# Kernel optimization log

Measured on AMD Instinct MI355X. Metric: run time of the kernel, lower is better.

## Reference

```python
import jax, jax.numpy as jnp
import numpy as np

GROUPS = 8   # GroupNorm groups used by create_pat_conv*_blocks(..., groups=8)
EPS = 1e-5
K = 20       # num_neighbor


def group_norm(x, gamma, beta):
    # x: [B, C, ...spatial]
    B, C = x.shape[0], x.shape[1]
    shape = x.shape
    xg = x.reshape(B, GROUPS, C // GROUPS, -1)
    m = xg.mean(axis=(2, 3), keepdims=True)
    v = ((xg - m) ** 2).mean(axis=(2, 3), keepdims=True)
    xg = (xg - m) * jax.lax.rsqrt(v + EPS)
    x = xg.reshape(shape)
    bshape = (1, C) + (1,) * (len(shape) - 2)
    return x * gamma.reshape(bshape) + beta.reshape(bshape)


def conv_block(x, w, b, gamma, beta):
    # pointwise (kernel-size 1) conv + GroupNorm + ELU, works for 1d and 2d spatial
    y = jnp.einsum('oc,bc...->bo...', w, x) + b.reshape((1, -1) + (1,) * (x.ndim - 2))
    return jax.nn.elu(group_norm(y, gamma, beta))


def knn_graph(points, k):
    # points: [B, 3, N] -> neighbor coords [B, 3, N, k] (self included, dilation=1)
    sq = jnp.sum(points * points, axis=1)                      # [B, N]
    inner = jnp.einsum('bci,bcj->bij', points, points)         # [B, N, N]
    dist = sq[:, :, None] + sq[:, None, :] - 2.0 * inner       # squared pairwise dist
    _, idx = jax.lax.top_k(-dist, k)                           # [B, N, k] smallest dists
    neighbors = jnp.take_along_axis(points[:, :, None, :], idx[:, None, :, :], axis=3)
    return neighbors                                           # [B, 3, N, k]


def setup_inputs() -> dict:
    key = jax.random.key(0)
    B, N = 4, 8192
    dims1 = [6, 32, 64]
    dims2 = [64, 512, 1024]
    keys = iter(jax.random.split(key, 32))
    inp = {"points": jax.random.normal(next(keys), (B, 3, N), dtype=jnp.float32)}
    for tag, dims in (("p1", dims1), ("p2", dims2)):
        for i in range(len(dims) - 1):
            cin, cout = dims[i], dims[i + 1]
            inp[f"{tag}_w{i}"] = jax.random.normal(next(keys), (cout, cin), dtype=jnp.float32) / np.float32(np.sqrt(cin))
            inp[f"{tag}_b{i}"] = jnp.zeros((cout,), dtype=jnp.float32)
            inp[f"{tag}_g{i}"] = jnp.ones((cout,), dtype=jnp.float32)
            inp[f"{tag}_beta{i}"] = jnp.zeros((cout,), dtype=jnp.float32)
    return inp


def reference(points, p1_w0, p1_b0, p1_g0, p1_beta0, p1_w1, p1_b1, p1_g1, p1_beta1,
              p2_w0, p2_b0, p2_g0, p2_beta0, p2_w1, p2_b1, p2_g1, p2_beta1):
    neighbors = knn_graph(points, K)                             # [B, 3, N, K]
    center = jnp.broadcast_to(points[:, :, :, None], neighbors.shape)
    x = jnp.concatenate([center, neighbors - center], axis=1)   # [B, 6, N, K]
    x = conv_block(x, p1_w0, p1_b0, p1_g0, p1_beta0)            # [B, 32, N, K]
    x = conv_block(x, p1_w1, p1_b1, p1_g1, p1_beta1)            # [B, 64, N, K]
    x = jnp.max(x, axis=2)                                      # [B, 64, K] (faithful to source: max over dim=2)
    x = conv_block(x, p2_w0, p2_b0, p2_g0, p2_beta0)            # [B, 512, K]
    x = conv_block(x, p2_w1, p2_b1, p2_g1, p2_beta1)            # [B, 1024, K]
    return x
```

## Files before the change

### kernel.cpp

```cpp
#include <hip/hip_runtime.h>
#include <math.h>

#define NPTS   8192
#define BATCH  4
#define KNN    20
#define NKTOT  (NPTS*KNN)
#define EPS    1e-5f
#define QC2    16

#define WINW   3072
#define WITR   (WINW/4/128)
#define NBIN   1024
#define BIN_LO (-4.5f)
#define BIN_W  (9.0f/1024.0f)

typedef float v2f __attribute__((ext_vector_type(2)));

__device__ __forceinline__ float elu(float x) { return x > 0.0f ? x : expm1f(x); }
__device__ __forceinline__ float eluf(float x) { return x > 0.0f ? x : __expf(x) - 1.0f; }
__device__ __forceinline__ v2f splat2(float x) { v2f v; v.x = x; v.y = x; return v; }
__device__ __forceinline__ float rfl(float x) {
    return __uint_as_float(__builtin_amdgcn_readfirstlane(__float_as_uint(x)));
}

__device__ __forceinline__ unsigned fenc(float f) {
    unsigned b = __float_as_uint(f);
    return b ^ ((unsigned)(((int)b) >> 31) | 0x80000000u);
}
__device__ __forceinline__ float fdec(unsigned u) {
    unsigned b = (u & 0x80000000u) ? (u ^ 0x80000000u) : ~u;
    return __uint_as_float(b);
}

__device__ __forceinline__ int xbin(float x) {
    int bin = (int)floorf((x + 4.5f) * (1024.0f / 9.0f));
    return bin < 0 ? 0 : (bin > NBIN - 1 ? NBIN - 1 : bin);
}

__global__ __launch_bounds__(256) void prep_kernel(const float* __restrict__ points,
                                                   float4* __restrict__ pts4,
                                                   float* __restrict__ zeroreg,
                                                   unsigned* __restrict__ minenc,
                                                   unsigned* __restrict__ fcnt)
{
    const int t = blockIdx.x * 256 + threadIdx.x;
    const int b = t >> 13, n = t & (NPTS - 1);
    const float* px = points + b * 3 * NPTS;
    float x = px[n], y = px[NPTS + n], z = px[2 * NPTS + n];
    pts4[t] = make_float4(x, y, z, -0.5f * (x * x + y * y + z * z));
    if (t < 18176) zeroreg[t] = 0.f;
    if (t < 5120)  minenc[t] = 0xFFFFFFFFu;
    if (t < 4)     fcnt[t] = 0u;
}

__global__ __launch_bounds__(1024) void hist_kernel(const float* __restrict__ points,
                                                    int* __restrict__ Pcur)
{
    __shared__ int h[NBIN];
    __shared__ int sc[NBIN];
    const int b = blockIdx.x;
    const int t = threadIdx.x;
    h[t] = 0;
    __syncthreads();
    const float* px = points + b * 3 * NPTS;
    for (int i = t; i < NPTS; i += 1024)
        atomicAdd(&h[xbin(px[i])], 1);
    __syncthreads();
    int v = h[t];
    sc[t] = v;
    __syncthreads();
    for (int off = 1; off < NBIN; off <<= 1) {
        int a = (t >= off) ? sc[t - off] : 0;
        __syncthreads();
        sc[t] += a;
        __syncthreads();
    }
    Pcur[b * NBIN + t] = sc[t] - v;
}

__global__ __launch_bounds__(256) void scatter_kernel(const float4* __restrict__ pts4,
                                                      int* __restrict__ Pcur,
                                                      float4* __restrict__ psort,
                                                      int* __restrict__ sidx,
                                                      int* __restrict__ binof)
{
    const int t = blockIdx.x * 256 + threadIdx.x;
    const int b = t >> 13, n = t & (NPTS - 1);
    float4 p = pts4[t];
    int bin = xbin(p.x);
    int slot = atomicAdd(&Pcur[b * NBIN + bin], 1);
    psort[b * NPTS + slot] = p;
    sidx [b * NPTS + slot] = n;
    binof[b * NPTS + slot] = bin;
}

__global__ __launch_bounds__(256, 8) void knn_win_kernel(
    const float4* __restrict__ psort, const int* __restrict__ sidx,
    const int* __restrict__ binof, int* __restrict__ idx_out,
    unsigned* __restrict__ fcnt, int* __restrict__ flist)
{
    __shared__ unsigned long long queue[32][QC2];
    __shared__ float smaxs[4][8][64];
    __shared__ float gates[8];
    __shared__ int qcnt[32];

    const int tid  = threadIdx.x;
    const int lane = tid & 63;
    const int wv   = tid >> 6;
    const int b    = blockIdx.x >> 10;
    const int oct  = blockIdx.x & 1023;
    const int q0s  = oct * 8;
    const float4* psb = psort + b * NPTS;
    const int*    six = sidx  + b * NPTS;
    const int*    bob = binof + b * NPTS;

    int s = q0s + 4 - WINW / 2;
    if (s < 0) s = 0;
    if (s > NPTS - WINW) s = NPTS - WINW;

    if (tid < 32) qcnt[tid] = 0;

    float qx[8], qy[8], qz[8], q2[8];
    v2f smax2[8];
#pragma unroll
    for (int q = 0; q < 8; ++q) {
        float4 qp = psb[q0s + q];
        qx[q] = rfl(qp.x); qy[q] = rfl(qp.y); qz[q] = rfl(qp.z);
        q2[q] = rfl(-(qp.w + qp.w));
        smax2[q] = splat2(-INFINITY);
    }

    const int lbase = s + wv * 2 + lane * 8;

#pragma unroll 3
    for (int t = 0; t < WITR; ++t) {
        float4 p0 = psb[lbase + t * 512];
        float4 p1 = psb[lbase + t * 512 + 1];
        v2f px = { p0.x, p1.x }, py = { p0.y, p1.y };
        v2f pz = { p0.z, p1.z }, pw = { p0.w, p1.w };
#pragma unroll
        for (int q = 0; q < 8; ++q) {
            v2f sv = __builtin_elementwise_fma(splat2(qx[q]), px,
                     __builtin_elementwise_fma(splat2(qy[q]), py,
                     __builtin_elementwise_fma(splat2(qz[q]), pz, pw)));
            smax2[q] = __builtin_elementwise_max(smax2[q], sv);
        }
    }
#pragma unroll
    for (int q = 0; q < 8; ++q) smaxs[wv][q][lane] = fmaxf(smax2[q].x, smax2[q].y);
    __syncthreads();

#pragma unroll
    for (int qq = 0; qq < 2; ++qq) {
        const int q = wv * 2 + qq;
        float v = fmaxf(fmaxf(smaxs[0][q][lane], smaxs[1][q][lane]),
                        fmaxf(smaxs[2][q][lane], smaxs[3][q][lane]));
#pragma unroll
        for (int k = 2; k <= 64; k <<= 1)
#pragma unroll
            for (int j = k >> 1; j >= 1; j >>= 1) {
                float o = __shfl_xor(v, j);
                bool up = ((lane & k) == 0);
                bool keepmin = (((lane & j) == 0) == up);
                v = keepmin ? fminf(v, o) : fmaxf(v, o);
            }
        float m = __shfl(v, 44);
        if (lane == 0) gates[q] = m - 1e-4f - 1e-5f * fabsf(m);
    }
    __syncthreads();
    float sgate[8];
#pragma unroll
    for (int q = 0; q < 8; ++q) sgate[q] = gates[q];

    for (int t = 0; t < WITR; ++t) {
        const int jb = lbase + t * 512;
        float4 p0 = psb[jb];
        float4 p1 = psb[jb + 1];
        v2f px = { p0.x, p1.x }, py = { p0.y, p1.y };
        v2f pz = { p0.z, p1.z }, pw = { p0.w, p1.w };
#pragma unroll
        for (int q = 0; q < 8; ++q) {
            v2f sv = __builtin_elementwise_fma(splat2(qx[q]), px,
                     __builtin_elementwise_fma(splat2(qy[q]), py,
                     __builtin_elementwise_fma(splat2(qz[q]), pz, pw)));
            if (fmaxf(sv.x, sv.y) >= sgate[q]) {
#pragma unroll
                for (int h = 0; h < 2; ++h) {
                    float svh = h ? sv.y : sv.x;
                    if (svh >= sgate[q]) {
                        int slot = atomicAdd(&qcnt[wv * 8 + q], 1);
                        if (slot < QC2) {
                            int j = six[jb + h];
                            queue[wv * 8 + q][slot] =
                                ((unsigned long long)fenc(svh) << 32)
                                | (unsigned)(NPTS - 1 - j);
                        }
                    }
                }
            }
        }
    }
    __syncthreads();

    float xLe = (s == 0) ? -3.0e38f
                         : (BIN_LO + (float)(bob[s] + 1) * BIN_W);
    float xRe = (s == NPTS - WINW) ? 3.0e38f
                         : (BIN_LO + (float)bob[s + WINW] * BIN_W);

#pragma unroll
    for (int qq = 0; qq < 2; ++qq) {
        const int q = wv * 2 + qq;
        int c0r = qcnt[0 * 8 + q], c1r = qcnt[1 * 8 + q];
        int c2r = qcnt[2 * 8 + q], c3r = qcnt[3 * 8 + q];
        const bool ovf = (c0r > QC2) || (c1r > QC2) || (c2r > QC2) || (c3r > QC2);
        int c0 = c0r < QC2 ? c0r : QC2;
        int c1 = c1r < QC2 ? c1r : QC2;
        int c2 = c2r < QC2 ? c2r : QC2;
        int c3 = c3r < QC2 ? c3r : QC2;
        int b1 = c0, b2 = c0 + c1, b3 = c0 + c1 + c2, b4 = b3 + c3;
        unsigned long long key = 0ull;
        if (lane < b1)      key = queue[0 * 8 + q][lane];
        else if (lane < b2) key = queue[1 * 8 + q][lane - b1];
        else if (lane < b3) key = queue[2 * 8 + q][lane - b2];
        else if (lane < b4) key = queue[3 * 8 + q][lane - b3];
#pragma unroll
        for (int k = 2; k <= 64; k <<= 1)
#pragma unroll
            for (int j = k >> 1; j >= 1; j >>= 1) {
                unsigned long long o = __shfl_xor(key, j);
                bool up = ((lane & k) == 0);
                bool keepmax = (((lane & j) == 0) == up);
                bool omax = o > key;
                key = (keepmax == omax) ? o : key;
            }
        const int oq = __builtin_amdgcn_readfirstlane(six[q0s + q]);
        if (lane < KNN)
            idx_out[(b * KNN + lane) * NPTS + oq] =
                NPTS - 1 - (int)(unsigned)(key & 0xFFFFFFFFu);

        unsigned long long k19 = __shfl(key, 19);
        float s20 = fdec((unsigned)(k19 >> 32));
        float d20 = fmaxf(q2[q] - 2.0f * s20, 0.0f);
        float mg  = 1e-3f + 1e-3f * d20;
        float dL  = qx[q] - xLe;
        float dR  = xRe - qx[q];
        bool ok = !ovf && dL > 0.0f && dR > 0.0f
                  && (d20 + mg < dL * dL) && (d20 + mg < dR * dR);
        if (!ok && lane == 0) {
            unsigned fs = atomicAdd(&fcnt[b], 1u);
            if (fs < 8192u) flist[b * 8192 + fs] = oq;
        }
    }
}

__global__ __launch_bounds__(256, 8) void knn_fb_kernel(const float4* __restrict__ pts4,
                                                        int* __restrict__ idx_out,
                                                        const unsigned* __restrict__ fcnt,
                                                        const int* __restrict__ flist)
{
    __shared__ unsigned long long queue[32][QC2];
    __shared__ float smaxs[4][8][64];
    __shared__ float gates[8];
    __shared__ int qcnt[32];

    const int tid  = threadIdx.x;
    const int lane = tid & 63;
    const int wv   = tid >> 6;
    const int bb   = blockIdx.x & 3;
    unsigned cnt = fcnt[bb];
    if (cnt > 8192u) cnt = 8192u;
    const float4* pb = pts4 + bb * NPTS;
    const int* fl = flist + bb * 8192;
    const int cbase = wv * (NPTS / 4);
    const int tstep = gridDim.x >> 2;

    for (int task = blockIdx.x >> 2; task * 8 < (int)cnt; task += tstep) {
        int qn8[8];
        float qx[8], qy[8], qz[8];
        v2f smax2[8];
        if (tid < 32) qcnt[tid] = 0;
#pragma unroll
        for (int q = 0; q < 8; ++q) {
            int e = task * 8 + q;
            if (e >= (int)cnt) e = (int)cnt - 1;
            qn8[q] = __builtin_amdgcn_readfirstlane(fl[e]);
            float4 qp = pb[qn8[q]];
            qx[q] = rfl(qp.x); qy[q] = rfl(qp.y); qz[q] = rfl(qp.z);
            smax2[q] = splat2(-INFINITY);
        }

#pragma unroll 4
        for (int t = 0; t < NPTS / 4 / 128; ++t) {
            float4 p0 = pb[cbase + t * 128 + 2 * lane];
            float4 p1 = pb[cbase + t * 128 + 2 * lane + 1];
            v2f px = { p0.x, p1.x }, py = { p0.y, p1.y };
            v2f pz = { p0.z, p1.z }, pw = { p0.w, p1.w };
#pragma unroll
            for (int q = 0; q < 8; ++q) {
                v2f sv = __builtin_elementwise_fma(splat2(qx[q]), px,
                         __builtin_elementwise_fma(splat2(qy[q]), py,
                         __builtin_elementwise_fma(splat2(qz[q]), pz, pw)));
                smax2[q] = __builtin_elementwise_max(smax2[q], sv);
            }
        }
#pragma unroll
        for (int q = 0; q < 8; ++q) smaxs[wv][q][lane] = fmaxf(smax2[q].x, smax2[q].y);
        __syncthreads();

#pragma unroll
        for (int qq = 0; qq < 2; ++qq) {
            const int q = wv * 2 + qq;
            float v = fmaxf(fmaxf(smaxs[0][q][lane], smaxs[1][q][lane]),
                            fmaxf(smaxs[2][q][lane], smaxs[3][q][lane]));
#pragma unroll
            for (int k = 2; k <= 64; k <<= 1)
#pragma unroll
                for (int j = k >> 1; j >= 1; j >>= 1) {
                    float o = __shfl_xor(v, j);
                    bool up = ((lane & k) == 0);
                    bool keepmin = (((lane & j) == 0) == up);
                    v = keepmin ? fminf(v, o) : fmaxf(v, o);
                }
            float m = __shfl(v, 44);
            if (lane == 0) gates[q] = m - 1e-4f - 1e-5f * fabsf(m);
        }
        __syncthreads();
        float sgate[8];
#pragma unroll
        for (int q = 0; q < 8; ++q) sgate[q] = gates[q];

        for (int t = 0; t < NPTS / 4 / 128; ++t) {
            float4 p0 = pb[cbase + t * 128 + 2 * lane];
            float4 p1 = pb[cbase + t * 128 + 2 * lane + 1];
            v2f px = { p0.x, p1.x }, py = { p0.y, p1.y };
            v2f pz = { p0.z, p1.z }, pw = { p0.w, p1.w };
            const int jb = cbase + t * 128 + 2 * lane;
#pragma unroll
            for (int q = 0; q < 8; ++q) {
                v2f sv = __builtin_elementwise_fma(splat2(qx[q]), px,
                         __builtin_elementwise_fma(splat2(qy[q]), py,
                         __builtin_elementwise_fma(splat2(qz[q]), pz, pw)));
                if (fmaxf(sv.x, sv.y) >= sgate[q]) {
#pragma unroll
                    for (int h = 0; h < 2; ++h) {
                        float svh = h ? sv.y : sv.x;
                        if (svh >= sgate[q]) {
                            int slot = atomicAdd(&qcnt[wv * 8 + q], 1);
                            if (slot < QC2) {
                                unsigned long long key =
                                    ((unsigned long long)fenc(svh) << 32)
                                    | (unsigned)(NPTS - 1 - (jb + h));
                                queue[wv * 8 + q][slot] = key;
                            }
                        }
                    }
                }
            }
        }
        __syncthreads();

#pragma unroll
        for (int qq = 0; qq < 2; ++qq) {
            const int q = wv * 2 + qq;
            int c0 = qcnt[0 * 8 + q];  c0 = c0 < QC2 ? c0 : QC2;
            int c1 = qcnt[1 * 8 + q];  c1 = c1 < QC2 ? c1 : QC2;
            int c2 = qcnt[2 * 8 + q];  c2 = c2 < QC2 ? c2 : QC2;
            int c3 = qcnt[3 * 8 + q];  c3 = c3 < QC2 ? c3 : QC2;
            int b1 = c0, b2 = c0 + c1, b3 = c0 + c1 + c2, b4 = b3 + c3;
            unsigned long long key = 0ull;
            if (lane < b1)      key = queue[0 * 8 + q][lane];
            else if (lane < b2) key = queue[1 * 8 + q][lane - b1];
            else if (lane < b3) key = queue[2 * 8 + q][lane - b2];
            else if (lane < b4) key = queue[3 * 8 + q][lane - b3];
#pragma unroll
            for (int k = 2; k <= 64; k <<= 1)
#pragma unroll
                for (int j = k >> 1; j >= 1; j >>= 1) {
                    unsigned long long o = __shfl_xor(key, j);
                    bool up = ((lane & k) == 0);
                    bool keepmax = (((lane & j) == 0) == up);
                    bool omax = o > key;
                    key = (keepmax == omax) ? o : key;
                }
            if (lane < KNN)
                idx_out[(bb * KNN + lane) * NPTS + qn8[q]] =
                    NPTS - 1 - (int)(unsigned)(key & 0xFFFFFFFFu);
        }
        __syncthreads();
    }
}

__global__ __launch_bounds__(256) void moments_x_kernel(const float4* __restrict__ pts4,
                                                        const int* __restrict__ idx,
                                                        float* __restrict__ sums1p)
{
    const int b  = blockIdx.x / 80;
    const int r0 = (blockIdx.x - b * 80) * 2048;
    const float4* pb = pts4 + b * NPTS;
    const int* ib = idx + b * NKTOT;

    float v[27];
#pragma unroll
    for (int i = 0; i < 27; ++i) v[i] = 0.f;

    for (int e = 0; e < 8; ++e) {
        const int id = r0 + e * 256 + threadIdx.x;
        const int n = id & (NPTS - 1);
        const int j = ib[id];
        float4 c4 = pb[n];
        float4 e4 = pb[j];
        float x[6] = { c4.x, c4.y, c4.z, e4.x - c4.x, e4.y - c4.y, e4.z - c4.z };
        int p = 6;
#pragma unroll
        for (int d = 0; d < 6; ++d) {
            v[d] += x[d];
#pragma unroll
            for (int ee = d; ee < 6; ++ee) v[p++] += x[d] * x[ee];
        }
    }
#pragma unroll
    for (int i = 0; i < 27; ++i)
        for (int o = 32; o > 0; o >>= 1) v[i] += __shfl_xor(v[i], o);

    __shared__ float red[4][27];
    const int lane = threadIdx.x & 63, w = threadIdx.x >> 6;
    if (lane == 0)
#pragma unroll
        for (int i = 0; i < 27; ++i) red[w][i] = v[i];
    __syncthreads();
    if (threadIdx.x < 27) {
        float acc = red[0][threadIdx.x] + red[1][threadIdx.x] + red[2][threadIdx.x] + red[3][threadIdx.x];
        int slot = blockIdx.x & 63;
        atomicAdd(&sums1p[(slot * BATCH + b) * 27 + threadIdx.x], acc);
    }
}

__global__ void finalize1_kernel(const float* __restrict__ sums1p,
                                 const float* __restrict__ w1, const float* __restrict__ b1,
                                 const float* __restrict__ g1, const float* __restrict__ beta1,
                                 float* __restrict__ w1f)
{
    __shared__ float S[BATCH][27];
    const int t = threadIdx.x;
    if (t < 108) {
        int b = t / 27, i = t % 27;
        float acc = 0.f;
        for (int s = 0; s < 64; ++s) acc += sums1p[(s * BATCH + b) * 27 + i];
        S[b][i] = acc;
    }
    __syncthreads();
    const int b = t >> 5, c = t & 31;
    const float invS = 1.0f / (float)NKTOT;
    float Ex[6], M[6][6];
#pragma unroll
    for (int d = 0; d < 6; ++d) Ex[d] = S[b][d] * invS;
    int p = 6;
#pragma unroll
    for (int d = 0; d < 6; ++d)
#pragma unroll
        for (int e = d; e < 6; ++e) { float v = S[b][p++] * invS; M[d][e] = v; M[e][d] = v; }
    const int g = c >> 2;
    float msum = 0.f, qsum = 0.f;
    for (int cc = g * 4; cc < g * 4 + 4; ++cc) {
        float w[6];
#pragma unroll
        for (int d = 0; d < 6; ++d) w[d] = w1[cc * 6 + d];
        float dotEx = 0.f;
#pragma unroll
        for (int d = 0; d < 6; ++d) dotEx += w[d] * Ex[d];
        float Ey = dotEx + b1[cc];
        float Ey2 = 0.f;
#pragma unroll
        for (int d = 0; d < 6; ++d)
#pragma unroll
            for (int e = 0; e < 6; ++e) Ey2 += w[d] * w[e] * M[d][e];
        Ey2 += 2.0f * b1[cc] * dotEx + b1[cc] * b1[cc];
        msum += Ey; qsum += Ey2;
    }
    float m = msum * 0.25f;
    float var = qsum * 0.25f - m * m;
    float inv = rsqrtf(var + EPS);
    float s = g1[c] * inv;
    float tt = s * (b1[c] - m) + beta1[c];
    float* o = w1f + (b * 32 + c) * 8;
#pragma unroll
    for (int d = 0; d < 6; ++d) o[d] = s * w1[c * 6 + d];
    o[6] = tt; o[7] = 0.f;
}

__global__ __launch_bounds__(256, 3) void fused_main_kernel(
    const float4* __restrict__ pts4, const int* __restrict__ idxb,
    const float* __restrict__ w1f, const float* __restrict__ w2, const float* __restrict__ b2,
    float* __restrict__ sums2p, unsigned int* __restrict__ maxenc, unsigned int* __restrict__ minenc)
{
    __shared__ __align__(16) float w2t[32 * 64];
    __shared__ __align__(16) float z1s[32 * 256];
    __shared__ __align__(16) float4 w1s4[64];
    __shared__ float b2s[64];
    __shared__ float redmx[256], redmn[256], sqred[64];

    const int t   = threadIdx.x;
    const int blk = blockIdx.x;
    const int nc  = blk & 15;
    const int k   = (blk >> 4) % 20;
    const int b   = blk / 320;

    for (int i = t; i < 512; i += 256) {
        float4 v = ((const float4*)w2)[i];
        int c = i >> 3, kq = (i & 7) * 4;
        w2t[(kq + 0) * 64 + c] = v.x; w2t[(kq + 1) * 64 + c] = v.y;
        w2t[(kq + 2) * 64 + c] = v.z; w2t[(kq + 3) * 64 + c] = v.w;
    }
    if (t < 64) { w1s4[t] = ((const float4*)w1f)[b * 64 + t]; b2s[t] = b2[t]; }

    const int wvi = t >> 6;
    const int cg8 = t & 7;
    const int n0  = (t >> 3) * 8;
    const int c0  = cg8 * 8;
    const float4* pb = pts4 + b * NPTS;
    const int nbase = nc * 512;
    const int* idxrow = idxb + (b * KNN + k) * NPTS;

    float mx[8], mn[8];
#pragma unroll
    for (int ci = 0; ci < 8; ++ci) { mx[ci] = -INFINITY; mn[ci] = INFINITY; }
    float gs = 0.f, gq = 0.f;

    for (int ph = 0; ph < 2; ++ph) {
        const int n = nbase + ph * 256 + t;
        const int j = idxrow[n];
        float4 c4 = pb[n];
        float4 e4 = pb[j];
        float x0[6] = { c4.x, c4.y, c4.z, e4.x - c4.x, e4.y - c4.y, e4.z - c4.z };

        __syncthreads();
#pragma unroll
        for (int c = 0; c < 32; ++c) {
            float4 wA = w1s4[c * 2 + 0];
            float4 wB = w1s4[c * 2 + 1];
            float z = wB.z;
            z = fmaf(wA.x, x0[0], z); z = fmaf(wA.y, x0[1], z); z = fmaf(wA.z, x0[2], z);
            z = fmaf(wA.w, x0[3], z); z = fmaf(wB.x, x0[4], z); z = fmaf(wB.y, x0[5], z);
            z1s[c * 256 + t] = eluf(z);
        }
        __syncthreads();

        float acc[8][8];
#pragma unroll
        for (int ci = 0; ci < 8; ++ci) {
            float bb = b2s[c0 + ci];
#pragma unroll
            for (int pj = 0; pj < 8; ++pj) acc[ci][pj] = bb;
        }
#pragma unroll
        for (int kk = 0; kk < 32; ++kk) {
            float4 a0 = *(const float4*)&w2t[kk * 64 + c0];
            float4 a1 = *(const float4*)&w2t[kk * 64 + c0 + 4];
            float4 z0 = *(const float4*)&z1s[kk * 256 + n0];
            float4 z1v = *(const float4*)&z1s[kk * 256 + n0 + 4];
            float avv[8] = { a0.x, a0.y, a0.z, a0.w, a1.x, a1.y, a1.z, a1.w };
            float zvv[8] = { z0.x, z0.y, z0.z, z0.w, z1v.x, z1v.y, z1v.z, z1v.w };
#pragma unroll
            for (int ci = 0; ci < 8; ++ci)
#pragma unroll
                for (int pj = 0; pj < 8; ++pj) acc[ci][pj] = fmaf(avv[ci], zvv[pj], acc[ci][pj]);
        }
#pragma unroll
        for (int ci = 0; ci < 8; ++ci)
#pragma unroll
            for (int pj = 0; pj < 8; ++pj) {
                float v = acc[ci][pj];
                gs += v; gq = fmaf(v, v, gq);
                mx[ci] = fmaxf(mx[ci], v); mn[ci] = fminf(mn[ci], v);
            }
    }

#pragma unroll
    for (int m = 8; m <= 32; m <<= 1) {
#pragma unroll
        for (int ci = 0; ci < 8; ++ci) {
            mx[ci] = fmaxf(mx[ci], __shfl_xor(mx[ci], m));
            mn[ci] = fminf(mn[ci], __shfl_xor(mn[ci], m));
        }
        gs += __shfl_xor(gs, m);
        gq += __shfl_xor(gq, m);
    }
    if ((t & 63) < 8) {
        const int l = t & 7;
#pragma unroll
        for (int ci = 0; ci < 8; ++ci) {
            redmx[wvi * 64 + l * 8 + ci] = mx[ci];
            redmn[wvi * 64 + l * 8 + ci] = mn[ci];
        }
        sqred[(wvi * 8 + l) * 2 + 0] = gs;
        sqred[(wvi * 8 + l) * 2 + 1] = gq;
    }
    __syncthreads();
    if (t < 64) {
        float m = fmaxf(fmaxf(redmx[t], redmx[64 + t]), fmaxf(redmx[128 + t], redmx[192 + t]));
        atomicMax(&maxenc[(b * 64 + t) * KNN + k], fenc(m));
    } else if (t < 128) {
        int c = t - 64;
        float m = fminf(fminf(redmn[c], redmn[64 + c]), fminf(redmn[128 + c], redmn[192 + c]));
        atomicMin(&minenc[(b * 64 + c) * KNN + k], fenc(m));
    } else if (t < 144) {
        int i2 = t - 128, g = i2 >> 1, w = i2 & 1;
        float v = 0.f;
#pragma unroll
        for (int wv2 = 0; wv2 < 4; ++wv2)
            v += sqred[(wv2 * 8 + g) * 2 + w];
        int slot = blk & 63;
        atomicAdd(&sums2p[((slot * BATCH + b) * 8 + g) * 2 + w], v);
    }
}

__global__ void build_m1_kernel(const float* __restrict__ sums2p,
                                const unsigned int* __restrict__ maxenc,
                                const unsigned int* __restrict__ minenc,
                                const float* __restrict__ gamma, const float* __restrict__ beta,
                                float* __restrict__ m1)
{
    const int t = blockIdx.x * 256 + threadIdx.x;
    const int b = t / 1280;
    const int r = t - b * 1280;
    const int c = r / 20;
    const int g = c >> 3;
    float s = 0.f, q = 0.f;
    for (int sl = 0; sl < 64; ++sl) {
        s += sums2p[((sl * BATCH + b) * 8 + g) * 2 + 0];
        q += sums2p[((sl * BATCH + b) * 8 + g) * 2 + 1];
    }
    const float cnt = 8.0f * (float)NKTOT;
    float m = s / cnt;
    float var = q / cnt - m * m;
    float inv = rsqrtf(var + EPS);
    float sc = gamma[c] * inv;
    float tt = beta[c] - sc * m;
    float y = (sc >= 0.f) ? fdec(maxenc[t]) : fdec(minenc[t]);
    m1[t] = elu(sc * y + tt);
}

template <int CIN, int SLOTS>
__global__ void p2_gemm_kernel(const float* __restrict__ zin, const float* __restrict__ w,
                               const float* __restrict__ bias, float* __restrict__ yout,
                               float* __restrict__ sumsp, int chans_per_group)
{
    const int t = blockIdx.x * 256 + threadIdx.x;
    const int per_b = (gridDim.x * 256) / BATCH;
    const int b = t / per_b;
    const int r = t - b * per_b;
    const int o = r / 20;
    const int k = r - o * 20;
    const float* zb = zin + b * CIN * 20;
    const float* wrow = w + o * CIN;
    float acc = bias[o];
    for (int c = 0; c < CIN; c += 4) {
        float4 wv = *(const float4*)&wrow[c];
        acc += wv.x * zb[(c + 0) * 20 + k] + wv.y * zb[(c + 1) * 20 + k]
             + wv.z * zb[(c + 2) * 20 + k] + wv.w * zb[(c + 3) * 20 + k];
    }
    yout[t] = acc;

    __shared__ float ls[16];
    if (threadIdx.x < 16) ls[threadIdx.x] = 0.f;
    __syncthreads();
    const int g = o / chans_per_group;
    atomicAdd(&ls[g * 2 + 0], acc);
    atomicAdd(&ls[g * 2 + 1], acc * acc);
    __syncthreads();
    if (threadIdx.x < 16) {
        int slot = blockIdx.x & (SLOTS - 1);
        atomicAdd(&sumsp[(slot * BATCH + b) * 16 + threadIdx.x], ls[threadIdx.x]);
    }
}

template <int SLOTS>
__global__ void p2_finalize_kernel(const float* __restrict__ y, const float* __restrict__ sumsp,
                                   const float* __restrict__ gamma, const float* __restrict__ beta,
                                   float* __restrict__ z, int chans_per_group, float cnt)
{
    const int t = blockIdx.x * 256 + threadIdx.x;
    const int per_b = (gridDim.x * 256) / BATCH;
    const int b = t / per_b;
    const int r = t - b * per_b;
    const int o = r / 20;
    const int g = o / chans_per_group;
    float s = 0.f, q = 0.f;
    for (int sl = 0; sl < SLOTS; ++sl) {
        s += sumsp[(sl * BATCH + b) * 16 + g * 2 + 0];
        q += sumsp[(sl * BATCH + b) * 16 + g * 2 + 1];
    }
    float m = s / cnt;
    float var = q / cnt - m * m;
    float inv = rsqrtf(var + EPS);
    float v = gamma[o] * inv * (y[t] - m) + beta[o];
    z[t] = elu(v);
}

extern "C" void kernel_launch(void* const* d_in, const int* in_sizes, int n_in,
                              void* d_out, int out_size, void* d_ws, size_t ws_size,
                              hipStream_t stream)
{
    const float* points  = (const float*)d_in[0];
    const float* p1_w0   = (const float*)d_in[1];
    const float* p1_b0   = (const float*)d_in[2];
    const float* p1_g0   = (const float*)d_in[3];
    const float* p1_bt0  = (const float*)d_in[4];
    const float* p1_w1   = (const float*)d_in[5];
    const float* p1_b1   = (const float*)d_in[6];
    const float* p1_g1   = (const float*)d_in[7];
    const float* p1_bt1  = (const float*)d_in[8];
    const float* p2_w0   = (const float*)d_in[9];
    const float* p2_b0   = (const float*)d_in[10];
    const float* p2_g0   = (const float*)d_in[11];
    const float* p2_bt0  = (const float*)d_in[12];
    const float* p2_w1   = (const float*)d_in[13];
    const float* p2_b1   = (const float*)d_in[14];
    const float* p2_g1   = (const float*)d_in[15];
    const float* p2_bt1  = (const float*)d_in[16];
    float* out = (float*)d_out;

    float* ws = (float*)d_ws;
    int*      idx     = (int*)ws;
    float*    sums1p  = ws + 655360;
    float*    sums2p  = sums1p + 6912;
    float*    sumsAp  = sums2p + 4096;
    float*    sumsBp  = sumsAp + 1024;
    unsigned* maxenc  = (unsigned*)(sumsBp + 1024);
    unsigned* minenc  = maxenc + 5120;
    float*    w1f     = (float*)(minenc + 5120);
    float*    m1      = w1f + 1024;
    float*    yp2a    = m1 + 5120;
    float*    zp2a    = yp2a + 40960;
    float*    yp2b    = zp2a + 40960;
    float4*   pts4    = (float4*)yp2a;
    float*    psortf  = yp2b + 81920;
    float4*   psort4  = (float4*)psortf;
    int*      sidx    = (int*)(psortf + 131072);
    int*      binof   = sidx + 32768;
    int*      Pcur    = binof + 32768 + 64;
    unsigned* fcnt4   = (unsigned*)(Pcur + 4096);
    int*      flist   = (int*)(fcnt4 + 64);

    prep_kernel<<<128, 256, 0, stream>>>(points, pts4, sums1p, minenc, fcnt4);
    hist_kernel<<<4, 1024, 0, stream>>>(points, Pcur);
    scatter_kernel<<<128, 256, 0, stream>>>(pts4, Pcur, psort4, sidx, binof);
    knn_win_kernel<<<4096, 256, 0, stream>>>(psort4, sidx, binof, idx, fcnt4, flist);
    knn_fb_kernel<<<1024, 256, 0, stream>>>(pts4, idx, fcnt4, flist);
    moments_x_kernel<<<320, 256, 0, stream>>>(pts4, idx, sums1p);
    finalize1_kernel<<<1, 128, 0, stream>>>(sums1p, p1_w0, p1_b0, p1_g0, p1_bt0, w1f);
    fused_main_kernel<<<1280, 256, 0, stream>>>(pts4, idx, w1f, p1_w1, p1_b1,
                                                sums2p, maxenc, minenc);
    build_m1_kernel<<<20, 256, 0, stream>>>(sums2p, maxenc, minenc, p1_g1, p1_bt1, m1);
    p2_gemm_kernel<64, 16><<<160, 256, 0, stream>>>(m1, p2_w0, p2_b0, yp2a, sumsAp, 64);
    p2_finalize_kernel<16><<<160, 256, 0, stream>>>(yp2a, sumsAp, p2_g0, p2_bt0, zp2a, 64, 1280.0f);
    p2_gemm_kernel<512, 16><<<320, 256, 0, stream>>>(zp2a, p2_w1, p2_b1, yp2b, sumsBp, 128);
    p2_finalize_kernel<16><<<320, 256, 0, stream>>>(yp2b, sumsBp, p2_g1, p2_bt1, out, 128, 2560.0f);
}
```

Measured before the change: 297.7 us.

## Keep KNN indices in sorted point order and gather from sorted points downstream

KNN results are now stored as slot indices into the x-sorted point array, with the original index kept only as a tie-break in the sort key. The moments and fused main kernels gather centers and neighbors from the sorted buffer, relying on the later max over points and the GroupNorm statistics being permutation-invariant. Spatially close neighbors become close in memory, which is meant to improve gather locality. The fallback kernel is also reshaped to 2 queries per block with a single 64-entry queue, 4096 blocks and an early exit, and the window kernel's lane-to-point mapping changes.

```diff
diff --git a/kernel.cpp b/kernel.cpp
--- a/kernel.cpp
+++ b/kernel.cpp
@@ -7,6 +7,7 @@
 #define NKTOT  (NPTS*KNN)
 #define EPS    1e-5f
 #define QC2    16
+#define FQC    64
 
 #define WINW   3072
 #define WITR   (WINW/4/128)
@@ -35,6 +36,11 @@
 __device__ __forceinline__ int xbin(float x) {
     int bin = (int)floorf((x + 4.5f) * (1024.0f / 9.0f));
     return bin < 0 ? 0 : (bin > NBIN - 1 ? NBIN - 1 : bin);
+}
+
+__device__ __forceinline__ unsigned long long packkey(float s, int orig, int slot) {
+    return ((unsigned long long)fenc(s) << 32)
+         | (unsigned)(((NPTS - 1 - orig) << 13) | slot);
 }
 
 __global__ __launch_bounds__(256) void prep_kernel(const float* __restrict__ points,
@@ -130,7 +136,7 @@
         smax2[q] = splat2(-INFINITY);
     }
 
-    const int lbase = s + wv * 2 + lane * 8;
+    const int lbase = s + (((lane >> 5) * 4 + wv) << 6) + ((lane & 31) << 1);
 
 #pragma unroll 3
     for (int t = 0; t < WITR; ++t) {
@@ -189,12 +195,8 @@
                     float svh = h ? sv.y : sv.x;
                     if (svh >= sgate[q]) {
                         int slot = atomicAdd(&qcnt[wv * 8 + q], 1);
-                        if (slot < QC2) {
-                            int j = six[jb + h];
-                            queue[wv * 8 + q][slot] =
-                                ((unsigned long long)fenc(svh) << 32)
-                                | (unsigned)(NPTS - 1 - j);
-                        }
+                        if (slot < QC2)
+                            queue[wv * 8 + q][slot] = packkey(svh, six[jb + h], jb + h);
                     }
                 }
             }
@@ -233,10 +235,9 @@
                 bool omax = o > key;
                 key = (keepmax == omax) ? o : key;
             }
-        const int oq = __builtin_amdgcn_readfirstlane(six[q0s + q]);
         if (lane < KNN)
-            idx_out[(b * KNN + lane) * NPTS + oq] =
-                NPTS - 1 - (int)(unsigned)(key & 0xFFFFFFFFu);
+            idx_out[(b * KNN + lane) * NPTS + (q0s + q)] =
+                (int)(unsigned)(key & 0x1FFFu);
 
         unsigned long long k19 = __shfl(key, 19);
         float s20 = fdec((unsigned)(k19 >> 32));
@@ -248,20 +249,21 @@
                   && (d20 + mg < dL * dL) && (d20 + mg < dR * dR);
         if (!ok && lane == 0) {
             unsigned fs = atomicAdd(&fcnt[b], 1u);
-            if (fs < 8192u) flist[b * 8192 + fs] = oq;
-        }
-    }
-}
-
-__global__ __launch_bounds__(256, 8) void knn_fb_kernel(const float4* __restrict__ pts4,
+            if (fs < 8192u) flist[b * 8192 + fs] = q0s + q;
+        }
+    }
+}
+
+__global__ __launch_bounds__(256, 8) void knn_fb_kernel(const float4* __restrict__ psort,
+                                                        const int* __restrict__ sidx,
                                                         int* __restrict__ idx_out,
                                                         const unsigned* __restrict__ fcnt,
                                                         const int* __restrict__ flist)
 {
-    __shared__ unsigned long long queue[32][QC2];
-    __shared__ float smaxs[4][8][64];
-    __shared__ float gates[8];
-    __shared__ int qcnt[32];
+    __shared__ unsigned long long queue[2][FQC];
+    __shared__ float smaxs[4][2][64];
+    __shared__ float gates[2];
+    __shared__ int qcnt[2];
 
     const int tid  = threadIdx.x;
     const int lane = tid & 63;
@@ -269,22 +271,24 @@
     const int bb   = blockIdx.x & 3;
     unsigned cnt = fcnt[bb];
     if (cnt > 8192u) cnt = 8192u;
-    const float4* pb = pts4 + bb * NPTS;
+    if (cnt == 0u) return;
+    const float4* pb = psort + bb * NPTS;
+    const int* six = sidx + bb * NPTS;
     const int* fl = flist + bb * 8192;
     const int cbase = wv * (NPTS / 4);
     const int tstep = gridDim.x >> 2;
 
-    for (int task = blockIdx.x >> 2; task * 8 < (int)cnt; task += tstep) {
-        int qn8[8];
-        float qx[8], qy[8], qz[8];
-        v2f smax2[8];
-        if (tid < 32) qcnt[tid] = 0;
-#pragma unroll
-        for (int q = 0; q < 8; ++q) {
-            int e = task * 8 + q;
+    for (int task = blockIdx.x >> 2; task * 2 < (int)cnt; task += tstep) {
+        int qs[2];
+        float qx[2], qy[2], qz[2];
+        v2f smax2[2];
+        if (tid < 2) qcnt[tid] = 0;
+#pragma unroll
+        for (int q = 0; q < 2; ++q) {
+            int e = task * 2 + q;
             if (e >= (int)cnt) e = (int)cnt - 1;
-            qn8[q] = __builtin_amdgcn_readfirstlane(fl[e]);
-            float4 qp = pb[qn8[q]];
+            qs[q] = __builtin_amdgcn_readfirstlane(fl[e]);
+            float4 qp = pb[qs[q]];
             qx[q] = rfl(qp.x); qy[q] = rfl(qp.y); qz[q] = rfl(qp.z);
             smax2[q] = splat2(-INFINITY);
         }
@@ -296,7 +300,7 @@
             v2f px = { p0.x, p1.x }, py = { p0.y, p1.y };
             v2f pz = { p0.z, p1.z }, pw = { p0.w, p1.w };
 #pragma unroll
-            for (int q = 0; q < 8; ++q) {
+            for (int q = 0; q < 2; ++q) {
                 v2f sv = __builtin_elementwise_fma(splat2(qx[q]), px,
                          __builtin_elementwise_fma(splat2(qy[q]), py,
                          __builtin_elementwise_fma(splat2(qz[q]), pz, pw)));
@@ -304,12 +308,11 @@
             }
         }
 #pragma unroll
-        for (int q = 0; q < 8; ++q) smaxs[wv][q][lane] = fmaxf(smax2[q].x, smax2[q].y);
+        for (int q = 0; q < 2; ++q) smaxs[wv][q][lane] = fmaxf(smax2[q].x, smax2[q].y);
         __syncthreads();
 
-#pragma unroll
-        for (int qq = 0; qq < 2; ++qq) {
-            const int q = wv * 2 + qq;
+        if (wv < 2) {
+            const int q = wv;
             float v = fmaxf(fmaxf(smaxs[0][q][lane], smaxs[1][q][lane]),
                             fmaxf(smaxs[2][q][lane], smaxs[3][q][lane]));
 #pragma unroll
@@ -325,33 +328,28 @@
             if (lane == 0) gates[q] = m - 1e-4f - 1e-5f * fabsf(m);
         }
         __syncthreads();
-        float sgate[8];
-#pragma unroll
-        for (int q = 0; q < 8; ++q) sgate[q] = gates[q];
+        float sg0 = gates[0], sg1 = gates[1];
 
         for (int t = 0; t < NPTS / 4 / 128; ++t) {
-            float4 p0 = pb[cbase + t * 128 + 2 * lane];
-            float4 p1 = pb[cbase + t * 128 + 2 * lane + 1];
+            const int jb = cbase + t * 128 + 2 * lane;
+            float4 p0 = pb[jb];
+            float4 p1 = pb[jb + 1];
             v2f px = { p0.x, p1.x }, py = { p0.y, p1.y };
             v2f pz = { p0.z, p1.z }, pw = { p0.w, p1.w };
-            const int jb = cbase + t * 128 + 2 * lane;
-#pragma unroll
-            for (int q = 0; q < 8; ++q) {
+#pragma unroll
+            for (int q = 0; q < 2; ++q) {
+                float sg = q ? sg1 : sg0;
                 v2f sv = __builtin_elementwise_fma(splat2(qx[q]), px,
                          __builtin_elementwise_fma(splat2(qy[q]), py,
                          __builtin_elementwise_fma(splat2(qz[q]), pz, pw)));
-                if (fmaxf(sv.x, sv.y) >= sgate[q]) {
+                if (fmaxf(sv.x, sv.y) >= sg) {
 #pragma unroll
                     for (int h = 0; h < 2; ++h) {
                         float svh = h ? sv.y : sv.x;
-                        if (svh >= sgate[q]) {
-                            int slot = atomicAdd(&qcnt[wv * 8 + q], 1);
-                            if (slot < QC2) {
-                                unsigned long long key =
-                                    ((unsigned long long)fenc(svh) << 32)
-                                    | (unsigned)(NPTS - 1 - (jb + h));
-                                queue[wv * 8 + q][slot] = key;
-                            }
+                        if (svh >= sg) {
+                            int slot = atomicAdd(&qcnt[q], 1);
+                            if (slot < FQC)
+                                queue[q][slot] = packkey(svh, six[jb + h], jb + h);
                         }
                     }
                 }
@@ -359,19 +357,10 @@
         }
         __syncthreads();
 
-#pragma unroll
-        for (int qq = 0; qq < 2; ++qq) {
-            const int q = wv * 2 + qq;
-            int c0 = qcnt[0 * 8 + q];  c0 = c0 < QC2 ? c0 : QC2;
-            int c1 = qcnt[1 * 8 + q];  c1 = c1 < QC2 ? c1 : QC2;
-            int c2 = qcnt[2 * 8 + q];  c2 = c2 < QC2 ? c2 : QC2;
-            int c3 = qcnt[3 * 8 + q];  c3 = c3 < QC2 ? c3 : QC2;
-            int b1 = c0, b2 = c0 + c1, b3 = c0 + c1 + c2, b4 = b3 + c3;
-            unsigned long long key = 0ull;
-            if (lane < b1)      key = queue[0 * 8 + q][lane];
-            else if (lane < b2) key = queue[1 * 8 + q][lane - b1];
-            else if (lane < b3) key = queue[2 * 8 + q][lane - b2];
-            else if (lane < b4) key = queue[3 * 8 + q][lane - b3];
+        if (wv < 2) {
+            const int q = wv;
+            int c = qcnt[q]; c = c < FQC ? c : FQC;
+            unsigned long long key = (lane < c) ? queue[q][lane] : 0ull;
 #pragma unroll
             for (int k = 2; k <= 64; k <<= 1)
 #pragma unroll
@@ -383,20 +372,20 @@
                     key = (keepmax == omax) ? o : key;
                 }
             if (lane < KNN)
-                idx_out[(bb * KNN + lane) * NPTS + qn8[q]] =
-                    NPTS - 1 - (int)(unsigned)(key & 0xFFFFFFFFu);
+                idx_out[(bb * KNN + lane) * NPTS + qs[q]] =
+                    (int)(unsigned)(key & 0x1FFFu);
         }
         __syncthreads();
     }
 }
 
-__global__ __launch_bounds__(256) void moments_x_kernel(const float4* __restrict__ pts4,
+__global__ __launch_bounds__(256) void moments_x_kernel(const float4* __restrict__ psort,
                                                         const int* __restrict__ idx,
                                                         float* __restrict__ sums1p)
 {
     const int b  = blockIdx.x / 80;
     const int r0 = (blockIdx.x - b * 80) * 2048;
-    const float4* pb = pts4 + b * NPTS;
+    const float4* pb = psort + b * NPTS;
     const int* ib = idx + b * NKTOT;
 
     float v[27];
@@ -489,7 +478,7 @@
 }
 
 __global__ __launch_bounds__(256, 3) void fused_main_kernel(
-    const float4* __restrict__ pts4, const int* __restrict__ idxb,
+    const float4* __restrict__ psort, const int* __restrict__ idxb,
     const float* __restrict__ w1f, const float* __restrict__ w2, const float* __restrict__ b2,
     float* __restrict__ sums2p, unsigned int* __restrict__ maxenc, unsigned int* __restrict__ minenc)
 {
@@ -517,7 +506,7 @@
     const int cg8 = t & 7;
     const int n0  = (t >> 3) * 8;
     const int c0  = cg8 * 8;
-    const float4* pb = pts4 + b * NPTS;
+    const float4* pb = psort + b * NPTS;
     const int nbase = nc * 512;
     const int* idxrow = idxb + (b * KNN + k) * NPTS;
 
@@ -746,10 +735,10 @@
     hist_kernel<<<4, 1024, 0, stream>>>(points, Pcur);
     scatter_kernel<<<128, 256, 0, stream>>>(pts4, Pcur, psort4, sidx, binof);
     knn_win_kernel<<<4096, 256, 0, stream>>>(psort4, sidx, binof, idx, fcnt4, flist);
-    knn_fb_kernel<<<1024, 256, 0, stream>>>(pts4, idx, fcnt4, flist);
-    moments_x_kernel<<<320, 256, 0, stream>>>(pts4, idx, sums1p);
+    knn_fb_kernel<<<4096, 256, 0, stream>>>(psort4, sidx, idx, fcnt4, flist);
+    moments_x_kernel<<<320, 256, 0, stream>>>(psort4, idx, sums1p);
     finalize1_kernel<<<1, 128, 0, stream>>>(sums1p, p1_w0, p1_b0, p1_g0, p1_bt0, w1f);
-    fused_main_kernel<<<1280, 256, 0, stream>>>(pts4, idx, w1f, p1_w1, p1_b1,
+    fused_main_kernel<<<1280, 256, 0, stream>>>(psort4, idx, w1f, p1_w1, p1_b1,
                                                 sums2p, maxenc, minenc);
     build_m1_kernel<<<20, 256, 0, stream>>>(sums2p, maxenc, minenc, p1_g1, p1_bt1, m1);
     p2_gemm_kernel<64, 16><<<160, 256, 0, stream>>>(m1, p2_w0, p2_b0, yp2a, sumsAp, 64);
```

Result: faster. 268.9 us (-9.7%).
